# Optimization experiments

Hardware: AMD Instinct MI355X
Metric: run time of the kernel (lower is better)

Reference implementation:

```python
import jax, jax.numpy as jnp
import numpy as np

SIGS = (0.08, 0.02)  # hardcoded sigmas from Varifold_loss.__init__
EPS = 1e-12


def _face_geom(V, F):
    # V: [nv,3] float, F: [nf,3] int -> centers [nf,3], areas [nf], unit normals [nf,3]
    v0, v1, v2 = V[F[:, 0]], V[F[:, 1]], V[F[:, 2]]
    C = (v0 + v1 + v2) / 3.0
    N = 0.5 * jnp.cross(v1 - v0, v2 - v0)  # area-weighted normal
    L = jnp.sqrt(jnp.sum(N * N, axis=-1) + EPS)  # triangle area
    return C, L, N / L[:, None]


def _inner(Cx, Lx, Nx, Cy, Ly, Ny, sigma):
    # unoriented squared-dot Gaussian varifold inner product: sum_ij Lx_i Ly_j exp(-|c_i-c_j|^2/s^2) (n_i.n_j)^2
    d2 = (Cx * Cx).sum(-1)[:, None] + (Cy * Cy).sum(-1)[None, :] - 2.0 * (Cx @ Cy.T)
    K = jnp.exp(-d2 / (sigma * sigma)) * (Nx @ Ny.T) ** 2  # [nfx, nfy]
    return Lx @ (K @ Ly)


def setup_inputs() -> dict:
    key = jax.random.key(0)
    k1, k2, k3, k4 = jax.random.split(key, 4)
    B, V, F = 1, 5023, 8000
    return {
        "predictions": jax.random.normal(k1, (B, V, 3), jnp.float32) * 0.1,
        "targets": jax.random.normal(k2, (B, V, 3), jnp.float32) * 0.1,
        "pred_faces": jax.random.randint(k3, (B, F, 3), 0, V),
        "target_faces": jax.random.randint(k4, (B, F, 3), 0, V),
    }


def reference(predictions, targets, pred_faces, target_faces):
    def per_item(V1, F1, V2, F2):
        C1, L1, N1 = _face_geom(V1, F1)
        C2, L2, N2 = _face_geom(V2, F2)
        total = jnp.float32(0.0)
        for s in SIGS:  # small fixed set of sigmas (structural loop)
            w = jnp.float32((s / SIGS[0]) ** 2)
            total = total + w * (
                _inner(C1, L1, N1, C1, L1, N1, s)
                + _inner(C2, L2, N2, C2, L2, N2, s)
                - 2.0 * _inner(C1, L1, N1, C2, L2, N2, s)
            )
        return total
    L = jax.vmap(per_item)(predictions, pred_faces, targets, target_faces)
    return jnp.mean(L)
```

## Files before the change

kernel.cpp:

```cpp
#include <hip/hip_runtime.h>

#define BLOCK 256
#define IR 4
#define JCHUNK 128

#define LN2 0.69314718055994530942
#define K1F ((float)(-1.0/(0.08*0.08*LN2)))
#define W2F 0.0625f


__global__ void geom_kernel(const float* __restrict__ vpred,
                            const float* __restrict__ vtarg,
                            const int* __restrict__ pf,
                            const int* __restrict__ tf,
                            float4* __restrict__ ws4,
                            float* __restrict__ out, int F)
{
    int id = blockIdx.x * blockDim.x + threadIdx.x;
    float diag = 0.0f;
    if (id < 2 * F) {
        int m = id / F;
        int f = id - m * F;
        const float* Vv = m ? vtarg : vpred;
        const int* Fc = m ? tf : pf;
        int i0 = Fc[3 * f + 0];
        int i1 = Fc[3 * f + 1];
        int i2 = Fc[3 * f + 2];
        float ax = Vv[3 * i0 + 0], ay = Vv[3 * i0 + 1], az = Vv[3 * i0 + 2];
        float bx = Vv[3 * i1 + 0], by = Vv[3 * i1 + 1], bz = Vv[3 * i1 + 2];
        float cx = Vv[3 * i2 + 0], cy = Vv[3 * i2 + 1], cz = Vv[3 * i2 + 2];

        const float third = 1.0f / 3.0f;
        float Cx = (ax + bx + cx) * third;
        float Cy = (ay + by + cy) * third;
        float Cz = (az + bz + cz) * third;

        float e1x = bx - ax, e1y = by - ay, e1z = bz - az;
        float e2x = cx - ax, e2y = cy - ay, e2z = cz - az;
        float Nx = 0.5f * (e1y * e2z - e1z * e2y);
        float Ny = 0.5f * (e1z * e2x - e1x * e2z);
        float Nz = 0.5f * (e1x * e2y - e1y * e2x);
        float nn = Nx * Nx + Ny * Ny + Nz * Nz;
        float L = sqrtf(nn + 1e-12f);
        float invSL = 1.0f / sqrtf(L);

        const float g = sqrtf(-2.0f * K1F);
        float c2 = Cx * Cx + Cy * Cy + Cz * Cz;
        ws4[m * F + f] = make_float4(g * Cx, g * Cy, g * Cz, K1F * c2);
        ws4[2 * F + m * F + f] = make_float4(Nx * invSL, Ny * invSL, Nz * invSL, 0.0f);

        float d = nn / L;
        diag = (1.0f + W2F) * d * d;
    }
    for (int off = 32; off > 0; off >>= 1) diag += __shfl_down(diag, off, 64);
    if ((threadIdx.x & 63) == 0 && diag != 0.0f) atomicAdd(out, diag);
}

#define JLOOP(PRED)                                                        \
    _Pragma("unroll 2")                                                    \
    for (int j = 0; j < jn; ++j) {                                         \
        float4 a = sJ[2 * j];                                              \
        float4 b = sJ[2 * j + 1];                                          \
        _Pragma("unroll")                                                  \
        for (int k = 0; k < IR; ++k) {                                     \
            float tt = s1i[k] + a.w;                                       \
            tt = fmaf(pxi[k], a.x, tt);                                    \
            tt = fmaf(pyi[k], a.y, tt);                                    \
            tt = fmaf(pzi[k], a.z, tt);                                    \
            float nd = mxi[k] * b.x;                                       \
            nd = fmaf(myi[k], b.y, nd);                                    \
            nd = fmaf(mzi[k], b.z, nd);                                    \
            float p = nd * nd;                                             \
            if (PRED) p = (j0 + j < ibase + k * BLOCK) ? p : 0.0f;         \
            float e1 = __builtin_amdgcn_exp2f(tt);                         \
            float e2 = __builtin_amdgcn_exp2f(tt * 16.0f);                 \
            accA[k] = fmaf(p, e1, accA[k]);                                \
            accB[k] = fmaf(p, e2, accB[k]);                                \
        }                                                                  \
    }

__launch_bounds__(BLOCK)
__global__ void pair_kernel(const float4* __restrict__ ws4,
                            float* __restrict__ out, int F,
                            int nJC, int nSym)
{
    const int q = (BLOCK * IR) / JCHUNK;
    const int iPerBlk = BLOCK * IR;

    int bid = blockIdx.x;
    int t, ib, jc;
    float coeff;
    bool predFlag = false;

    if (bid < 2 * nSym) {
        t = (bid < nSym) ? 0 : 1;
        int r = bid - t * nSym;
        int ibf = 0, off = 0;
        for (;;) {
            int c = (ibf + 1) * q;
            if (c > nJC) c = nJC;
            if (r < off + c) break;
            off += c;
            ibf++;
        }
        ib = ibf;
        jc = r - off;
        coeff = 2.0f;
        predFlag = (jc >= ib * q);
    } else {
        int r = bid - 2 * nSym;
        t = 2;
        ib = r / nJC;
        jc = r - ib * nJC;
        coeff = -2.0f;
    }

    int X = (t == 1) ? 1 : 0;
    int Y = (t == 0) ? 0 : 1;

    const float4* __restrict__ A_x = ws4 + X * F;
    const float4* __restrict__ B_x = ws4 + 2 * F + X * F;
    const float4* __restrict__ A_y = ws4 + Y * F;
    const float4* __restrict__ B_y = ws4 + 2 * F + Y * F;

    __shared__ float4 sJ[2 * JCHUNK];

    int tid = threadIdx.x;
    int j0 = jc * JCHUNK;
    int jn = (F - j0 < JCHUNK) ? (F - j0) : JCHUNK;
    for (int s = tid; s < jn; s += BLOCK) {
        sJ[2 * s] = A_y[j0 + s];
        sJ[2 * s + 1] = B_y[j0 + s];
    }
    __syncthreads();

    float pxi[IR], pyi[IR], pzi[IR], s1i[IR];
    float mxi[IR], myi[IR], mzi[IR];
    float accA[IR], accB[IR];
    int ibase = ib * iPerBlk + tid;
#pragma unroll
    for (int k = 0; k < IR; k++) {
        int i = ibase + k * BLOCK;
        float4 a = make_float4(0.f, 0.f, 0.f, 0.f);
        float4 b = make_float4(0.f, 0.f, 0.f, 0.f);
        if (i < F) { a = A_x[i]; b = B_x[i]; }
        pxi[k] = a.x; pyi[k] = a.y; pzi[k] = a.z; s1i[k] = a.w;
        mxi[k] = b.x; myi[k] = b.y; mzi[k] = b.z;
        accA[k] = 0.0f; accB[k] = 0.0f;
    }

    if (!predFlag) {
        JLOOP(false)
    } else {
        JLOOP(true)
    }

    float sA = 0.0f, sB = 0.0f;
#pragma unroll
    for (int k = 0; k < IR; k++) { sA += accA[k]; sB += accB[k]; }
    float ps = (sA + W2F * sB) * coeff;

    for (int off = 32; off > 0; off >>= 1) ps += __shfl_down(ps, off, 64);

    __shared__ float wsum[BLOCK / 64];
    int wid = tid >> 6;
    int lane = tid & 63;
    if (lane == 0) wsum[wid] = ps;
    __syncthreads();
    if (tid == 0) {
        float bs = 0.0f;
        for (int w = 0; w < BLOCK / 64; w++) bs += wsum[w];
        atomicAdd(out, bs);
    }
}

extern "C" void kernel_launch(void* const* d_in, const int* in_sizes, int n_in,
                              void* d_out, int out_size, void* d_ws, size_t ws_size,
                              hipStream_t stream) {
    const float* vpred = (const float*)d_in[0];
    const float* vtarg = (const float*)d_in[1];
    const int* pf = (const int*)d_in[2];
    const int* tf = (const int*)d_in[3];
    float* out = (float*)d_out;
    float4* ws4 = (float4*)d_ws;

    int F = in_sizes[2] / 3;

    hipMemsetAsync(out, 0, sizeof(float), stream);

    int gthreads = 2 * F;
    geom_kernel<<<(gthreads + BLOCK - 1) / BLOCK, BLOCK, 0, stream>>>(
        vpred, vtarg, pf, tf, ws4, out, F);

    int iPerBlk = BLOCK * IR;
    int nIB = (F + iPerBlk - 1) / iPerBlk;
    int nJC = (F + JCHUNK - 1) / JCHUNK;
    int q = iPerBlk / JCHUNK;
    int nSym = 0;
    for (int ib = 0; ib < nIB; ++ib) {
        int c = (ib + 1) * q;
        if (c > nJC) c = nJC;
        nSym += c;
    }
    int blocks = 2 * nSym + nIB * nJC;
    pair_kernel<<<blocks, BLOCK, 0, stream>>>(ws4, out, F, nJC, nSym);
}
```

Measured before the change: 126.5 us.

## Interleave face workspace, drop LDS staging, shrink pair blocks to 128 threads

The geometry workspace is now interleaved per face (center record next to normal record) instead of stored as separate arrays. The pair kernel no longer stages the j-chunk in shared memory with a barrier; each lane reads the uniform j entries directly from global memory, relying on the cache and scalar/broadcast loads. The pair block size drops to 128 threads (512 i per block), so the grid has more blocks, and the per-block LDS reduction becomes one atomic per wavefront. In exchange, the kernel issues more global atomics and depends on the cache serving the broadcast j loads.

```diff
diff --git a/kernel.cpp b/kernel.cpp
--- a/kernel.cpp
+++ b/kernel.cpp
@@ -1,11 +1,13 @@
 #include <hip/hip_runtime.h>
 
-#define BLOCK 256
+#define GBLOCK 256
+#define PBLOCK 128
 #define IR 4
 #define JCHUNK 128
+#define IPB (PBLOCK * IR)
 
 #define LN2 0.69314718055994530942
-#define K1F ((float)(-1.0/(0.08*0.08*LN2)))
+#define K1F ((float)(-1.0 / (0.08 * 0.08 * LN2)))
 #define W2F 0.0625f
 
 
@@ -19,7 +21,7 @@
     int id = blockIdx.x * blockDim.x + threadIdx.x;
     float diag = 0.0f;
     if (id < 2 * F) {
-        int m = id / F;
+        int m = (id >= F) ? 1 : 0;
         int f = id - m * F;
         const float* Vv = m ? vtarg : vpred;
         const int* Fc = m ? tf : pf;
@@ -46,32 +48,32 @@
 
         const float g = sqrtf(-2.0f * K1F);
         float c2 = Cx * Cx + Cy * Cy + Cz * Cz;
-        ws4[m * F + f] = make_float4(g * Cx, g * Cy, g * Cz, K1F * c2);
-        ws4[2 * F + m * F + f] = make_float4(Nx * invSL, Ny * invSL, Nz * invSL, 0.0f);
+        ws4[2 * id] = make_float4(g * Cx, g * Cy, g * Cz, K1F * c2);
+        ws4[2 * id + 1] = make_float4(Nx * invSL, Ny * invSL, Nz * invSL, 0.0f);
 
         float d = nn / L;
         diag = (1.0f + W2F) * d * d;
     }
     for (int off = 32; off > 0; off >>= 1) diag += __shfl_down(diag, off, 64);
-    if ((threadIdx.x & 63) == 0 && diag != 0.0f) atomicAdd(out, diag);
+    if ((threadIdx.x & 63) == 0) atomicAdd(out, diag);
 }
 
 #define JLOOP(PRED)                                                        \
     _Pragma("unroll 2")                                                    \
     for (int j = 0; j < jn; ++j) {                                         \
-        float4 a = sJ[2 * j];                                              \
-        float4 b = sJ[2 * j + 1];                                          \
+        const float4 aj = Wy[2 * (j0 + j)];                                \
+        const float4 bj = Wy[2 * (j0 + j) + 1];                            \
         _Pragma("unroll")                                                  \
         for (int k = 0; k < IR; ++k) {                                     \
-            float tt = s1i[k] + a.w;                                       \
-            tt = fmaf(pxi[k], a.x, tt);                                    \
-            tt = fmaf(pyi[k], a.y, tt);                                    \
-            tt = fmaf(pzi[k], a.z, tt);                                    \
-            float nd = mxi[k] * b.x;                                       \
-            nd = fmaf(myi[k], b.y, nd);                                    \
-            nd = fmaf(mzi[k], b.z, nd);                                    \
+            float tt = s1i[k] + aj.w;                                      \
+            tt = fmaf(pxi[k], aj.x, tt);                                   \
+            tt = fmaf(pyi[k], aj.y, tt);                                   \
+            tt = fmaf(pzi[k], aj.z, tt);                                   \
+            float nd = mxi[k] * bj.x;                                      \
+            nd = fmaf(myi[k], bj.y, nd);                                   \
+            nd = fmaf(mzi[k], bj.z, nd);                                   \
             float p = nd * nd;                                             \
-            if (PRED) p = (j0 + j < ibase + k * BLOCK) ? p : 0.0f;         \
+            if (PRED) p = (j0 + j < ibase + k * PBLOCK) ? p : 0.0f;        \
             float e1 = __builtin_amdgcn_exp2f(tt);                         \
             float e2 = __builtin_amdgcn_exp2f(tt * 16.0f);                 \
             accA[k] = fmaf(p, e1, accA[k]);                                \
@@ -79,14 +81,11 @@
         }                                                                  \
     }
 
-__launch_bounds__(BLOCK)
+__launch_bounds__(PBLOCK)
 __global__ void pair_kernel(const float4* __restrict__ ws4,
                             float* __restrict__ out, int F,
                             int nJC, int nSym)
 {
-    const int q = (BLOCK * IR) / JCHUNK;
-    const int iPerBlk = BLOCK * IR;
-
     int bid = blockIdx.x;
     int t, ib, jc;
     float coeff;
@@ -97,7 +96,7 @@
         int r = bid - t * nSym;
         int ibf = 0, off = 0;
         for (;;) {
-            int c = (ibf + 1) * q;
+            int c = 4 * (ibf + 1);
             if (c > nJC) c = nJC;
             if (r < off + c) break;
             off += c;
@@ -106,7 +105,7 @@
         ib = ibf;
         jc = r - off;
         coeff = 2.0f;
-        predFlag = (jc >= ib * q);
+        predFlag = (jc * JCHUNK + JCHUNK > ib * IPB);
     } else {
         int r = bid - 2 * nSym;
         t = 2;
@@ -117,33 +116,23 @@
 
     int X = (t == 1) ? 1 : 0;
     int Y = (t == 0) ? 0 : 1;
-
-    const float4* __restrict__ A_x = ws4 + X * F;
-    const float4* __restrict__ B_x = ws4 + 2 * F + X * F;
-    const float4* __restrict__ A_y = ws4 + Y * F;
-    const float4* __restrict__ B_y = ws4 + 2 * F + Y * F;
-
-    __shared__ float4 sJ[2 * JCHUNK];
+    const float4* __restrict__ Wx = ws4 + 2 * X * F;
+    const float4* __restrict__ Wy = ws4 + 2 * Y * F;
 
     int tid = threadIdx.x;
     int j0 = jc * JCHUNK;
     int jn = (F - j0 < JCHUNK) ? (F - j0) : JCHUNK;
-    for (int s = tid; s < jn; s += BLOCK) {
-        sJ[2 * s] = A_y[j0 + s];
-        sJ[2 * s + 1] = B_y[j0 + s];
-    }
-    __syncthreads();
 
     float pxi[IR], pyi[IR], pzi[IR], s1i[IR];
     float mxi[IR], myi[IR], mzi[IR];
     float accA[IR], accB[IR];
-    int ibase = ib * iPerBlk + tid;
+    int ibase = ib * IPB + tid;
 #pragma unroll
     for (int k = 0; k < IR; k++) {
-        int i = ibase + k * BLOCK;
+        int i = ibase + k * PBLOCK;
         float4 a = make_float4(0.f, 0.f, 0.f, 0.f);
         float4 b = make_float4(0.f, 0.f, 0.f, 0.f);
-        if (i < F) { a = A_x[i]; b = B_x[i]; }
+        if (i < F) { a = Wx[2 * i]; b = Wx[2 * i + 1]; }
         pxi[k] = a.x; pyi[k] = a.y; pzi[k] = a.z; s1i[k] = a.w;
         mxi[k] = b.x; myi[k] = b.y; mzi[k] = b.z;
         accA[k] = 0.0f; accB[k] = 0.0f;
@@ -161,17 +150,7 @@
     float ps = (sA + W2F * sB) * coeff;
 
     for (int off = 32; off > 0; off >>= 1) ps += __shfl_down(ps, off, 64);
-
-    __shared__ float wsum[BLOCK / 64];
-    int wid = tid >> 6;
-    int lane = tid & 63;
-    if (lane == 0) wsum[wid] = ps;
-    __syncthreads();
-    if (tid == 0) {
-        float bs = 0.0f;
-        for (int w = 0; w < BLOCK / 64; w++) bs += wsum[w];
-        atomicAdd(out, bs);
-    }
+    if ((tid & 63) == 0) atomicAdd(out, ps);
 }
 
 extern "C" void kernel_launch(void* const* d_in, const int* in_sizes, int n_in,
@@ -189,19 +168,17 @@
     hipMemsetAsync(out, 0, sizeof(float), stream);
 
     int gthreads = 2 * F;
-    geom_kernel<<<(gthreads + BLOCK - 1) / BLOCK, BLOCK, 0, stream>>>(
+    geom_kernel<<<(gthreads + GBLOCK - 1) / GBLOCK, GBLOCK, 0, stream>>>(
         vpred, vtarg, pf, tf, ws4, out, F);
 
-    int iPerBlk = BLOCK * IR;
-    int nIB = (F + iPerBlk - 1) / iPerBlk;
+    int nIB = (F + IPB - 1) / IPB;
     int nJC = (F + JCHUNK - 1) / JCHUNK;
-    int q = iPerBlk / JCHUNK;
     int nSym = 0;
     for (int ib = 0; ib < nIB; ++ib) {
-        int c = (ib + 1) * q;
+        int c = 4 * (ib + 1);
         if (c > nJC) c = nJC;
         nSym += c;
     }
     int blocks = 2 * nSym + nIB * nJC;
-    pair_kernel<<<blocks, BLOCK, 0, stream>>>(ws4, out, F, nJC, nSym);
+    pair_kernel<<<blocks, PBLOCK, 0, stream>>>(ws4, out, F, nJC, nSym);
 }
```

After: 159.9 us. 1.26x slower.
